# Kernel tuning notes

Hardware: AMD Instinct MI355X
Metric: run time of the kernel (lower is better)

The kernel has to match this reference:

```python
import jax, jax.numpy as jnp
import numpy as np

NUM_HEADS = 16


def setup_inputs() -> dict:
    key = jax.random.key(0)
    k1, k2, k3 = jax.random.split(key, 3)
    T, B, E = 2048, 2, 1024
    x = jax.random.normal(k1, (T, B, E), dtype=jnp.float32)
    in_proj_w = jax.random.normal(k2, (E, 3 * E), dtype=jnp.float32) * (E ** -0.5)
    in_proj_b = jnp.zeros((3 * E,), dtype=jnp.float32)
    out_w = jax.random.normal(k3, (E, E), dtype=jnp.float32) * (E ** -0.5)
    out_b = jnp.zeros((E,), dtype=jnp.float32)
    return {"x": x, "in_proj_w": in_proj_w, "in_proj_b": in_proj_b,
            "out_w": out_w, "out_b": out_b}


def reference(x, in_proj_w, in_proj_b, out_w, out_b):
    # x: (tgt_len, bsz, embed_dim) -- seq-first, self-attention (q is k is v)
    T, B, E = x.shape
    H = NUM_HEADS
    D = E // H
    scaling = D ** -0.5
    # packed in-projection: einsum('bne,ef->bnf') over (T,B,E)
    proj = jnp.einsum('tbe,ef->tbf', x, in_proj_w) + in_proj_b
    q, k, v = jnp.split(proj, 3, axis=-1)  # each (T, B, E)
    # reshape to (T, B*H, D) then transpose to (B*H, T, D)
    q = q.reshape(T, B * H, D).transpose(1, 0, 2)
    k = k.reshape(T, B * H, D).transpose(1, 0, 2)
    v = v.reshape(T, B * H, D).transpose(1, 0, 2)
    # full O(T^2) attention matrix, scaling applied after QK^T as in source
    attn = jnp.einsum('bie,bje->bij', q, k) * scaling  # (B*H, T, T)
    attn = jax.nn.softmax(attn, axis=-1)
    out = jnp.einsum('bij,bje->bie', attn, v)  # (B*H, T, D)
    # faithful to source: reshape directly (no head transpose-back)
    out = out.reshape(B, T, E)
    out = jnp.einsum('bte,ef->btf', out, out_w) + out_b
    return out
```

## Files before the change

kernel.cpp:

```cpp
#include <hip/hip_runtime.h>
#include <stdint.h>

#define TSEQ 2048
#define NB 2
#define EMB 1024
#define NHEAD 16
#define HDIM 64
#define QSCALE 0.18033688f

typedef __bf16 bf16x8 __attribute__((ext_vector_type(8)));
typedef __bf16 bf16x4 __attribute__((ext_vector_type(4)));
typedef float f32x4 __attribute__((ext_vector_type(4)));

__device__ __forceinline__ void gload_lds16(const void* g, void* lds) {
    __builtin_amdgcn_global_load_lds(
        (const __attribute__((address_space(1))) unsigned int*)g,
        (__attribute__((address_space(3))) unsigned int*)lds, 16, 0, 0);
}

__global__ __launch_bounds__(256) void cvt_x_kernel(
    const float* __restrict__ x, __bf16* __restrict__ xb)
{
    const size_t idx = ((size_t)blockIdx.x * 256 + threadIdx.x) * 4;
    float4 v = *(const float4*)(x + idx);
    bf16x4 o = { (__bf16)v.x, (__bf16)v.y, (__bf16)v.z, (__bf16)v.w };
    *(bf16x4*)(xb + idx) = o;
}

__global__ __launch_bounds__(256) void transpose_cvt_kernel(
    const float* __restrict__ w_in, const float* __restrict__ w_out,
    __bf16* __restrict__ wiT, __bf16* __restrict__ whT)
{
    __shared__ float tile[32][33];
    int bx = blockIdx.x;
    const int by = blockIdx.y;
    const float* src; __bf16* dst; int sn;
    if (bx < 96) { src = w_in;  dst = wiT; sn = 3072; }
    else         { bx -= 96; src = w_out; dst = whT; sn = 1024; }
    const int tx = threadIdx.x, ty = threadIdx.y;
    #pragma unroll
    for (int i = 0; i < 4; ++i)
        tile[ty + i * 8][tx] = src[(size_t)(by * 32 + ty + i * 8) * sn + bx * 32 + tx];
    __syncthreads();
    #pragma unroll
    for (int i = 0; i < 4; ++i) {
        float v = tile[tx][ty + i * 8];
        dst[(size_t)(bx * 32 + ty + i * 8) * 1024 + by * 32 + tx] = (__bf16)v;
    }
}

__global__ __launch_bounds__(256) void gemm_qkv_kernel(
    const __bf16* __restrict__ A, const __bf16* __restrict__ BT,
    const float* __restrict__ bias,
    __bf16* __restrict__ Oq, __bf16* __restrict__ Ok, __bf16* __restrict__ Ov)
{
    __shared__ __align__(16) __bf16 As[128 * 64];
    __shared__ __align__(16) __bf16 Bs[128 * 64];
    const int tid = threadIdx.x;
    const int wave = tid >> 6, lane = tid & 63;
    const int l16 = lane & 15, quad = lane >> 4;
    const int wm = wave >> 1, wn = wave & 1;
    const int m0 = blockIdx.y * 128, n0 = blockIdx.x * 128;

    f32x4 acc[4][4];
    #pragma unroll
    for (int mt = 0; mt < 4; ++mt)
        #pragma unroll
        for (int nt = 0; nt < 4; ++nt)
            #pragma unroll
            for (int r = 0; r < 4; ++r) acc[mt][nt][r] = 0.f;

    int smrow[4], schunk[4], sbase[4];
    #pragma unroll
    for (int i = 0; i < 4; ++i) {
        int linear = (wave * 4 + i) * 64 + lane;
        smrow[i] = linear >> 3;
        schunk[i] = (linear & 7) ^ (smrow[i] & 7);
        sbase[i] = (wave * 4 + i) * 512;
    }

    for (int k0 = 0; k0 < 1024; k0 += 64) {
        #pragma unroll
        for (int i = 0; i < 4; ++i) {
            gload_lds16(A + (size_t)(m0 + smrow[i]) * 1024 + k0 + schunk[i] * 8,
                        As + sbase[i]);
            gload_lds16(BT + (size_t)(n0 + smrow[i]) * 1024 + k0 + schunk[i] * 8,
                        Bs + sbase[i]);
        }
        __syncthreads();
        #pragma unroll
        for (int kk = 0; kk < 2; ++kk) {
            bf16x8 am[4], bn[4];
            #pragma unroll
            for (int mt = 0; mt < 4; ++mt) {
                int row = wm * 64 + mt * 16 + l16;
                int c = (kk * 4 + quad) ^ (row & 7);
                am[mt] = *(const bf16x8*)(As + row * 64 + c * 8);
            }
            #pragma unroll
            for (int nt = 0; nt < 4; ++nt) {
                int row = wn * 64 + nt * 16 + l16;
                int c = (kk * 4 + quad) ^ (row & 7);
                bn[nt] = *(const bf16x8*)(Bs + row * 64 + c * 8);
            }
            #pragma unroll
            for (int mt = 0; mt < 4; ++mt)
                #pragma unroll
                for (int nt = 0; nt < 4; ++nt)
                    acc[mt][nt] = __builtin_amdgcn_mfma_f32_16x16x32_bf16(
                        am[mt], bn[nt], acc[mt][nt], 0, 0, 0);
        }
        __syncthreads();
    }

    #pragma unroll
    for (int nt = 0; nt < 4; ++nt) {
        const int col = n0 + wn * 64 + nt * 16 + l16;
        const float bv = bias[col];
        const int sec = col >> 10, f = col & 1023;
        const int h = f >> 6, d = f & 63;
        #pragma unroll
        for (int mt = 0; mt < 4; ++mt)
            #pragma unroll
            for (int r = 0; r < 4; ++r) {
                const int row = m0 + wm * 64 + mt * 16 + quad * 4 + r;
                float v = acc[mt][nt][r] + bv;
                const int t = row >> 1, b = row & 1;
                const int bh = b * NHEAD + h;
                if (sec == 0)
                    Oq[((size_t)bh * TSEQ + t) * HDIM + d] = (__bf16)(v * QSCALE);
                else if (sec == 1)
                    Ok[((size_t)bh * TSEQ + t) * HDIM + d] = (__bf16)v;
                else
                    Ov[((size_t)bh * HDIM + d) * TSEQ + t] = (__bf16)v;
            }
    }
}

__global__ __launch_bounds__(256) void attn_mfma_kernel(
    const __bf16* __restrict__ Q, const __bf16* __restrict__ K,
    const __bf16* __restrict__ Vt,
    __bf16* __restrict__ O0, __bf16* __restrict__ O1,
    float* __restrict__ L0, float* __restrict__ L1)
{
    __shared__ __align__(16) __bf16 Ks[2][64 * 64];
    __shared__ __align__(16) __bf16 Vs[2][64 * 64];
    __shared__ __align__(16) __bf16 Ps[4][32 * 64];

    const int tid  = threadIdx.x;
    const int wave = tid >> 6;
    const int lane = tid & 63;
    const int l16  = lane & 15;
    const int quad = lane >> 4;
    const int bh   = blockIdx.y;
    const int z    = blockIdx.z;
    const int q0   = blockIdx.x * 128 + wave * 32;
    const int kbase0 = z * (TSEQ / 2);

    __bf16* __restrict__ Opart = z ? O1 : O0;
    float*  __restrict__ Lpart = z ? L1 : L0;

    bf16x8 qf[2][2];
    #pragma unroll
    for (int mq = 0; mq < 2; ++mq) {
        const __bf16* Qrow = Q + ((size_t)bh * TSEQ + q0 + mq * 16 + l16) * HDIM;
        qf[mq][0] = *(const bf16x8*)(Qrow + quad * 8);
        qf[mq][1] = *(const bf16x8*)(Qrow + 32 + quad * 8);
    }

    f32x4 Oacc[2][4];
    #pragma unroll
    for (int mq = 0; mq < 2; ++mq)
        #pragma unroll
        for (int dt = 0; dt < 4; ++dt)
            #pragma unroll
            for (int r = 0; r < 4; ++r) Oacc[mq][dt][r] = 0.f;
    float l_part[2] = {0.f, 0.f};

    const __bf16* Kbase = K + (size_t)bh * TSEQ * HDIM;
    const __bf16* Vbase = Vt + (size_t)bh * HDIM * TSEQ;

    int srow[2], schk[2];
    #pragma unroll
    for (int i = 0; i < 2; ++i) {
        const int s = wave * 2 + i;
        srow[i] = s * 8 + (lane >> 3);
        schk[i] = (lane & 7) ^ (srow[i] & 7);
    }

#define STAGE(buf, kt)                                                        \
    {                                                                         \
        _Pragma("unroll")                                                     \
        for (int i = 0; i < 2; ++i) {                                         \
            const int s = wave * 2 + i;                                       \
            gload_lds16(Kbase + (size_t)(kbase0 + (kt) * 64 + srow[i]) * HDIM \
                            + schk[i] * 8,                                    \
                        &Ks[buf][s * 512]);                                   \
            gload_lds16(Vbase + (size_t)srow[i] * TSEQ + kbase0 + (kt) * 64   \
                            + schk[i] * 8,                                    \
                        &Vs[buf][s * 512]);                                   \
        }                                                                     \
    }

    STAGE(0, 0);

    #pragma unroll 2
    for (int kt = 0; kt < TSEQ / 128; ++kt) {
        const int buf = kt & 1;
        __syncthreads();
        if (kt + 1 < TSEQ / 128) STAGE(buf ^ 1, kt + 1);

        bf16x8 kf[4][2];
        #pragma unroll
        for (int nt = 0; nt < 4; ++nt) {
            const int row = nt * 16 + l16;
            #pragma unroll
            for (int ch = 0; ch < 2; ++ch) {
                const int c = (quad + 4 * ch) ^ (row & 7);
                kf[nt][ch] = *(const bf16x8*)(&Ks[buf][row * 64 + c * 8]);
            }
        }
        bf16x8 vf[4][2];
        #pragma unroll
        for (int dt = 0; dt < 4; ++dt) {
            const int row = dt * 16 + l16;
            #pragma unroll
            for (int h = 0; h < 2; ++h) {
                const int c = (quad + 4 * h) ^ (row & 7);
                vf[dt][h] = *(const bf16x8*)(&Vs[buf][row * 64 + c * 8]);
            }
        }

        #pragma unroll
        for (int mq = 0; mq < 2; ++mq) {
            #pragma unroll
            for (int nt = 0; nt < 4; ++nt) {
                f32x4 s = {0.f, 0.f, 0.f, 0.f};
                s = __builtin_amdgcn_mfma_f32_16x16x32_bf16(kf[nt][0], qf[mq][0], s, 0, 0, 0);
                s = __builtin_amdgcn_mfma_f32_16x16x32_bf16(kf[nt][1], qf[mq][1], s, 0, 0, 0);
                float p0 = exp2f(s[0]), p1 = exp2f(s[1]);
                float p2 = exp2f(s[2]), p3 = exp2f(s[3]);
                l_part[mq] += (p0 + p1) + (p2 + p3);
                bf16x4 pk = { (__bf16)p0, (__bf16)p1, (__bf16)p2, (__bf16)p3 };
                const int prow = mq * 16 + l16;
                const int kidx = nt * 16 + quad * 4;
                const int pos = ((kidx >> 3) ^ (prow & 7)) * 8 + (kidx & 7);
                *(bf16x4*)(&Ps[wave][prow * 64 + pos]) = pk;
            }
        }

        bf16x8 pa[2][2];
        #pragma unroll
        for (int mq = 0; mq < 2; ++mq) {
            const int prow = mq * 16 + l16;
            #pragma unroll
            for (int h = 0; h < 2; ++h) {
                const int c = (quad + 4 * h) ^ (prow & 7);
                pa[mq][h] = *(const bf16x8*)(&Ps[wave][prow * 64 + c * 8]);
            }
        }

        #pragma unroll
        for (int mq = 0; mq < 2; ++mq)
            #pragma unroll
            for (int dt = 0; dt < 4; ++dt) {
                Oacc[mq][dt] = __builtin_amdgcn_mfma_f32_16x16x32_bf16(
                    pa[mq][0], vf[dt][0], Oacc[mq][dt], 0, 0, 0);
                Oacc[mq][dt] = __builtin_amdgcn_mfma_f32_16x16x32_bf16(
                    pa[mq][1], vf[dt][1], Oacc[mq][dt], 0, 0, 0);
            }
    }
#undef STAGE

    #pragma unroll
    for (int mq = 0; mq < 2; ++mq) {
        float v = l_part[mq];
        v += __shfl_xor(v, 16);
        v += __shfl_xor(v, 32);
        if (quad == 0)
            Lpart[(size_t)bh * TSEQ + q0 + mq * 16 + l16] = v;
    }

    const size_t base = ((size_t)bh * TSEQ + q0) * HDIM;
    #pragma unroll
    for (int mq = 0; mq < 2; ++mq)
        #pragma unroll
        for (int dt = 0; dt < 4; ++dt)
            #pragma unroll
            for (int r = 0; r < 4; ++r) {
                const size_t idx = base +
                    (size_t)(mq * 16 + quad * 4 + r) * HDIM + dt * 16 + l16;
                Opart[idx] = (__bf16)Oacc[mq][dt][r];
            }
}

__global__ __launch_bounds__(256) void normalize_kernel(
    const __bf16* __restrict__ O0, const __bf16* __restrict__ O1,
    const float* __restrict__ L0, const float* __restrict__ L1,
    __bf16* __restrict__ Ob)
{
    const size_t gid = (size_t)blockIdx.x * 256 + threadIdx.x;
    const size_t idx = gid * 8;
    const size_t qi = idx >> 6;
    const float inv = 1.f / (L0[qi] + L1[qi]);
    bf16x8 a = *(const bf16x8*)(O0 + idx);
    bf16x8 b = *(const bf16x8*)(O1 + idx);
    bf16x8 o;
    #pragma unroll
    for (int j = 0; j < 8; ++j)
        o[j] = (__bf16)(((float)a[j] + (float)b[j]) * inv);
    *(bf16x8*)(Ob + idx) = o;
}

__global__ __launch_bounds__(256) void gemm_out_kernel(
    const __bf16* __restrict__ A, const __bf16* __restrict__ BT,
    const float* __restrict__ bias, float* __restrict__ out)
{
    __shared__ __align__(16) __bf16 As[64 * 64];
    __shared__ __align__(16) __bf16 Bs[64 * 64];
    const int tid = threadIdx.x;
    const int wave = tid >> 6, lane = tid & 63;
    const int l16 = lane & 15, quad = lane >> 4;
    const int wm = wave >> 1, wn = wave & 1;
    const int m0 = blockIdx.y * 64, n0 = blockIdx.x * 64;

    f32x4 acc[2][2];
    #pragma unroll
    for (int mt = 0; mt < 2; ++mt)
        #pragma unroll
        for (int nt = 0; nt < 2; ++nt)
            #pragma unroll
            for (int r = 0; r < 4; ++r) acc[mt][nt][r] = 0.f;

    int srow[2], schk[2], sbase[2];
    #pragma unroll
    for (int i = 0; i < 2; ++i) {
        const int s = wave * 2 + i;
        srow[i] = s * 8 + (lane >> 3);
        schk[i] = (lane & 7) ^ (srow[i] & 7);
        sbase[i] = s * 512;
    }

    for (int k0 = 0; k0 < 1024; k0 += 64) {
        #pragma unroll
        for (int i = 0; i < 2; ++i) {
            gload_lds16(A + (size_t)(m0 + srow[i]) * 1024 + k0 + schk[i] * 8,
                        As + sbase[i]);
            gload_lds16(BT + (size_t)(n0 + srow[i]) * 1024 + k0 + schk[i] * 8,
                        Bs + sbase[i]);
        }
        __syncthreads();
        #pragma unroll
        for (int kk = 0; kk < 2; ++kk) {
            bf16x8 am[2], bn[2];
            #pragma unroll
            for (int mt = 0; mt < 2; ++mt) {
                int row = wm * 32 + mt * 16 + l16;
                int c = (kk * 4 + quad) ^ (row & 7);
                am[mt] = *(const bf16x8*)(As + row * 64 + c * 8);
            }
            #pragma unroll
            for (int nt = 0; nt < 2; ++nt) {
                int row = wn * 32 + nt * 16 + l16;
                int c = (kk * 4 + quad) ^ (row & 7);
                bn[nt] = *(const bf16x8*)(Bs + row * 64 + c * 8);
            }
            #pragma unroll
            for (int mt = 0; mt < 2; ++mt)
                #pragma unroll
                for (int nt = 0; nt < 2; ++nt)
                    acc[mt][nt] = __builtin_amdgcn_mfma_f32_16x16x32_bf16(
                        am[mt], bn[nt], acc[mt][nt], 0, 0, 0);
        }
        __syncthreads();
    }

    #pragma unroll
    for (int nt = 0; nt < 2; ++nt) {
        const int col = n0 + wn * 32 + nt * 16 + l16;
        const float bv = bias[col];
        #pragma unroll
        for (int mt = 0; mt < 2; ++mt)
            #pragma unroll
            for (int r = 0; r < 4; ++r) {
                const int row = m0 + wm * 32 + mt * 16 + quad * 4 + r;
                out[(size_t)row * 1024 + col] = acc[mt][nt][r] + bv;
            }
    }
}

extern "C" void kernel_launch(void* const* d_in, const int* in_sizes, int n_in,
                              void* d_out, int out_size, void* d_ws, size_t ws_size,
                              hipStream_t stream) {
    const float* x     = (const float*)d_in[0];
    const float* w_in  = (const float*)d_in[1];
    const float* b_in  = (const float*)d_in[2];
    const float* w_out = (const float*)d_in[3];
    const float* b_out = (const float*)d_in[4];
    float* out = (float*)d_out;

    const size_t M1 = (size_t)1024 * 1024;
    __bf16* ws  = (__bf16*)d_ws;
    __bf16* xb  = ws;
    __bf16* wiT = xb  + 4 * M1;
    __bf16* whT = wiT + 3 * M1;
    __bf16* Qb  = whT + 1 * M1;
    __bf16* Kb  = Qb  + 4 * M1;
    __bf16* Vt  = Kb  + 4 * M1;
    __bf16* O0  = Vt  + 4 * M1;
    __bf16* O1  = O0  + 4 * M1;
    float*  L0  = (float*)(O1 + 4 * M1);
    float*  L1  = L0 + 65536;
    __bf16* Ob  = xb;

    cvt_x_kernel<<<4096, 256, 0, stream>>>(x, xb);
    transpose_cvt_kernel<<<dim3(128, 32), dim3(32, 8), 0, stream>>>(
        w_in, w_out, wiT, whT);
    gemm_qkv_kernel<<<dim3(24, 32), 256, 0, stream>>>(
        xb, wiT, b_in, Qb, Kb, Vt);
    attn_mfma_kernel<<<dim3(16, 32, 2), 256, 0, stream>>>(
        Qb, Kb, Vt, O0, O1, L0, L1);
    normalize_kernel<<<2048, 256, 0, stream>>>(O0, O1, L0, L1, Ob);
    gemm_out_kernel<<<dim3(16, 64), 256, 0, stream>>>(
        Ob, whT, b_out, out);
}
```

Measured before the change: 228.3 us.

## Split attention keys four ways and single-buffer K to raise occupancy

Doubles the key-dimension split of the attention kernel from 2 to 4, so there are twice as many blocks with half the loop length each. The K tile becomes single-buffered, reloaded after an extra barrier once its fragments are in registers, and V fragments are now loaded from LDS per output tile just before use. Launch bounds request 4 blocks per CU. The aim is more parallelism and occupancy, at the cost of more partial outputs written and read by the normalize kernel (two of them stored in the output buffer) and an extra sync per iteration.

```diff
diff --git a/kernel.cpp b/kernel.cpp
--- a/kernel.cpp
+++ b/kernel.cpp
@@ -6,6 +6,8 @@
 #define EMB 1024
 #define NHEAD 16
 #define HDIM 64
+#define KSPLIT 4
+#define NT (TSEQ / KSPLIT / 64)
 #define QSCALE 0.18033688f
 
 typedef __bf16 bf16x8 __attribute__((ext_vector_type(8)));
@@ -137,13 +139,15 @@
     }
 }
 
-__global__ __launch_bounds__(256) void attn_mfma_kernel(
+__global__ __launch_bounds__(256, 4) void attn_mfma_kernel(
     const __bf16* __restrict__ Q, const __bf16* __restrict__ K,
     const __bf16* __restrict__ Vt,
     __bf16* __restrict__ O0, __bf16* __restrict__ O1,
-    float* __restrict__ L0, float* __restrict__ L1)
-{
-    __shared__ __align__(16) __bf16 Ks[2][64 * 64];
+    __bf16* __restrict__ O2, __bf16* __restrict__ O3,
+    float* __restrict__ L0, float* __restrict__ L1,
+    float* __restrict__ L2, float* __restrict__ L3)
+{
+    __shared__ __align__(16) __bf16 Ks[64 * 64];
     __shared__ __align__(16) __bf16 Vs[2][64 * 64];
     __shared__ __align__(16) __bf16 Ps[4][32 * 64];
 
@@ -155,10 +159,10 @@
     const int bh   = blockIdx.y;
     const int z    = blockIdx.z;
     const int q0   = blockIdx.x * 128 + wave * 32;
-    const int kbase0 = z * (TSEQ / 2);
-
-    __bf16* __restrict__ Opart = z ? O1 : O0;
-    float*  __restrict__ Lpart = z ? L1 : L0;
+    const int kbase0 = z * (TSEQ / KSPLIT);
+
+    __bf16* __restrict__ Opart = (z == 0) ? O0 : (z == 1) ? O1 : (z == 2) ? O2 : O3;
+    float*  __restrict__ Lpart = (z == 0) ? L0 : (z == 1) ? L1 : (z == 2) ? L2 : L3;
 
     bf16x8 qf[2][2];
     #pragma unroll
@@ -177,8 +181,8 @@
             for (int r = 0; r < 4; ++r) Oacc[mq][dt][r] = 0.f;
     float l_part[2] = {0.f, 0.f};
 
-    const __bf16* Kbase = K + (size_t)bh * TSEQ * HDIM;
-    const __bf16* Vbase = Vt + (size_t)bh * HDIM * TSEQ;
+    const __bf16* Kbase = K + ((size_t)bh * TSEQ + kbase0) * HDIM;
+    const __bf16* Vbase = Vt + (size_t)bh * HDIM * TSEQ + kbase0;
 
     int srow[2], schk[2];
     #pragma unroll
@@ -193,10 +197,10 @@
         _Pragma("unroll")                                                     \
         for (int i = 0; i < 2; ++i) {                                         \
             const int s = wave * 2 + i;                                       \
-            gload_lds16(Kbase + (size_t)(kbase0 + (kt) * 64 + srow[i]) * HDIM \
+            gload_lds16(Kbase + (size_t)((kt) * 64 + srow[i]) * HDIM          \
                             + schk[i] * 8,                                    \
-                        &Ks[buf][s * 512]);                                   \
-            gload_lds16(Vbase + (size_t)srow[i] * TSEQ + kbase0 + (kt) * 64   \
+                        Ks + s * 512);                                        \
+            gload_lds16(Vbase + (size_t)srow[i] * TSEQ + (kt) * 64            \
                             + schk[i] * 8,                                    \
                         &Vs[buf][s * 512]);                                   \
         }                                                                     \
@@ -204,11 +208,9 @@
 
     STAGE(0, 0);
 
-    #pragma unroll 2
-    for (int kt = 0; kt < TSEQ / 128; ++kt) {
+    for (int kt = 0; kt < NT; ++kt) {
         const int buf = kt & 1;
         __syncthreads();
-        if (kt + 1 < TSEQ / 128) STAGE(buf ^ 1, kt + 1);
 
         bf16x8 kf[4][2];
         #pragma unroll
@@ -217,19 +219,11 @@
             #pragma unroll
             for (int ch = 0; ch < 2; ++ch) {
                 const int c = (quad + 4 * ch) ^ (row & 7);
-                kf[nt][ch] = *(const bf16x8*)(&Ks[buf][row * 64 + c * 8]);
-            }
-        }
-        bf16x8 vf[4][2];
-        #pragma unroll
-        for (int dt = 0; dt < 4; ++dt) {
-            const int row = dt * 16 + l16;
-            #pragma unroll
-            for (int h = 0; h < 2; ++h) {
-                const int c = (quad + 4 * h) ^ (row & 7);
-                vf[dt][h] = *(const bf16x8*)(&Vs[buf][row * 64 + c * 8]);
-            }
-        }
+                kf[nt][ch] = *(const bf16x8*)(&Ks[row * 64 + c * 8]);
+            }
+        }
+        __syncthreads();
+        if (kt + 1 < NT) STAGE(buf ^ 1, kt + 1);
 
         #pragma unroll
         for (int mq = 0; mq < 2; ++mq) {
@@ -259,16 +253,24 @@
                 pa[mq][h] = *(const bf16x8*)(&Ps[wave][prow * 64 + c * 8]);
             }
         }
-
-        #pragma unroll
-        for (int mq = 0; mq < 2; ++mq)
-            #pragma unroll
-            for (int dt = 0; dt < 4; ++dt) {
+        #pragma unroll
+        for (int dt = 0; dt < 4; ++dt) {
+            const int row = dt * 16 + l16;
+            bf16x8 v0, v1;
+            {
+                const int c0 = quad ^ (row & 7);
+                const int c1 = (quad + 4) ^ (row & 7);
+                v0 = *(const bf16x8*)(&Vs[buf][row * 64 + c0 * 8]);
+                v1 = *(const bf16x8*)(&Vs[buf][row * 64 + c1 * 8]);
+            }
+            #pragma unroll
+            for (int mq = 0; mq < 2; ++mq) {
                 Oacc[mq][dt] = __builtin_amdgcn_mfma_f32_16x16x32_bf16(
-                    pa[mq][0], vf[dt][0], Oacc[mq][dt], 0, 0, 0);
+                    pa[mq][0], v0, Oacc[mq][dt], 0, 0, 0);
                 Oacc[mq][dt] = __builtin_amdgcn_mfma_f32_16x16x32_bf16(
-                    pa[mq][1], vf[dt][1], Oacc[mq][dt], 0, 0, 0);
-            }
+                    pa[mq][1], v1, Oacc[mq][dt], 0, 0, 0);
+            }
+        }
     }
 #undef STAGE
 
@@ -296,19 +298,24 @@
 
 __global__ __launch_bounds__(256) void normalize_kernel(
     const __bf16* __restrict__ O0, const __bf16* __restrict__ O1,
+    const __bf16* __restrict__ O2, const __bf16* __restrict__ O3,
     const float* __restrict__ L0, const float* __restrict__ L1,
+    const float* __restrict__ L2, const float* __restrict__ L3,
     __bf16* __restrict__ Ob)
 {
     const size_t gid = (size_t)blockIdx.x * 256 + threadIdx.x;
     const size_t idx = gid * 8;
     const size_t qi = idx >> 6;
-    const float inv = 1.f / (L0[qi] + L1[qi]);
+    const float inv = 1.f / (L0[qi] + L1[qi] + L2[qi] + L3[qi]);
     bf16x8 a = *(const bf16x8*)(O0 + idx);
     bf16x8 b = *(const bf16x8*)(O1 + idx);
+    bf16x8 c = *(const bf16x8*)(O2 + idx);
+    bf16x8 d = *(const bf16x8*)(O3 + idx);
     bf16x8 o;
     #pragma unroll
     for (int j = 0; j < 8; ++j)
-        o[j] = (__bf16)(((float)a[j] + (float)b[j]) * inv);
+        o[j] = (__bf16)((((float)a[j] + (float)b[j]) +
+                         ((float)c[j] + (float)d[j])) * inv);
     *(bf16x8*)(Ob + idx) = o;
 }
 
@@ -411,6 +418,10 @@
     __bf16* O1  = O0  + 4 * M1;
     float*  L0  = (float*)(O1 + 4 * M1);
     float*  L1  = L0 + 65536;
+    float*  L2  = L1 + 65536;
+    float*  L3  = L2 + 65536;
+    __bf16* O2  = (__bf16*)d_out;
+    __bf16* O3  = O2 + 4 * M1;
     __bf16* Ob  = xb;
 
     cvt_x_kernel<<<4096, 256, 0, stream>>>(x, xb);
@@ -418,9 +429,10 @@
         w_in, w_out, wiT, whT);
     gemm_qkv_kernel<<<dim3(24, 32), 256, 0, stream>>>(
         xb, wiT, b_in, Qb, Kb, Vt);
-    attn_mfma_kernel<<<dim3(16, 32, 2), 256, 0, stream>>>(
-        Qb, Kb, Vt, O0, O1, L0, L1);
-    normalize_kernel<<<2048, 256, 0, stream>>>(O0, O1, L0, L1, Ob);
+    attn_mfma_kernel<<<dim3(16, 32, KSPLIT), 256, 0, stream>>>(
+        Qb, Kb, Vt, O0, O1, O2, O3, L0, L1, L2, L3);
+    normalize_kernel<<<2048, 256, 0, stream>>>(
+        O0, O1, O2, O3, L0, L1, L2, L3, Ob);
     gemm_out_kernel<<<dim3(16, 64), 256, 0, stream>>>(
         Ob, whT, b_out, out);
 }
```

Measured after the change: 217.3 us. 1.05x faster.
